# Kernel tuning notes

Measured on AMD Instinct MI355X. Metric: run time of the kernel, lower is better.

Reference implementation:

```python
import jax, jax.numpy as jnp
import numpy as np

N_NODES = 16384   # n_nodes
N_LINKS = 8192    # batch of target links
D_EMB = 128       # embedding dim
EDGE_P = 0.004    # adjacency density -> avg degree ~65


def setup_inputs() -> dict:
    key = jax.random.key(0)
    k1, k2, k3 = jax.random.split(key, 3)
    adj = jax.random.bernoulli(k1, EDGE_P, (N_NODES, N_NODES))
    adj = adj | adj.T                      # symmetric graph
    adj = adj & ~jnp.eye(N_NODES, dtype=bool)  # no self loops
    links = jax.random.randint(k2, (N_LINKS, 2), 0, N_NODES)
    emb = jax.random.normal(k3, (N_NODES, D_EMB), dtype=jnp.float32)
    return {"targetLink": links, "adjacent": adj, "NodeEmbedding": emb}


def reference(targetLink, adjacent, NodeEmbedding):
    # targetLink: [B,2] int, adjacent: [N,N] bool, NodeEmbedding: [N,D] float
    i = targetLink[:, 0]
    j = targetLink[:, 1]
    emb_i = NodeEmbedding[i]               # [B,D] gather
    emb_j = NodeEmbedding[j]               # [B,D] gather
    product = emb_i * emb_j                # [B,D]
    # common-neighbor indicator: u is a CN of (i,j) iff adj[i,u] and adj[j,u]
    cn_mask = (adjacent[i] & adjacent[j]).astype(NodeEmbedding.dtype)  # [B,N]
    # sum of embeddings over common neighbors (fused gather-reduce)
    cn_sum = cn_mask @ NodeEmbedding       # [B,D]
    return jnp.concatenate([product, cn_sum], axis=-1)  # [B,2D]
```

## Files before the change

kernel.cpp:

```cpp
#include <hip/hip_runtime.h>

#define N_NODES 16384
#define D_EMB   128
#define LIST_CAP 1024

__global__ __launch_bounds__(256) void detect_layout_kernel(
    const unsigned int* __restrict__ words, int* __restrict__ flag)
{
    __shared__ int s_any;
    if (threadIdx.x == 0) s_any = 0;
    __syncthreads();
    int any = 0;
    for (int k = threadIdx.x; k < 16384; k += 256) {
        if (words[k] > 1u) any = 1;
    }
    if (any) atomicOr(&s_any, 1);
    __syncthreads();
    if (threadIdx.x == 0) *flag = s_any;
}

__global__ __launch_bounds__(256) void ncn_kernel(
    const int* __restrict__ links,
    const void* __restrict__ adjv,
    const float* __restrict__ emb,
    float* __restrict__ out,
    const int* __restrict__ flag,
    int n_links)
{
    const int link = blockIdx.x;
    if (link >= n_links) return;

    const int i = links[2 * link];
    const int j = links[2 * link + 1];

    __shared__ int s_list[LIST_CAP];
    __shared__ int s_count;
    if (threadIdx.x == 0) s_count = 0;
    __syncthreads();

    const int byte_layout = flag ? flag[0] : 1;

    if (byte_layout) {
        const uint4* rowi = reinterpret_cast<const uint4*>(
            (const unsigned char*)adjv + (size_t)i * N_NODES);
        const uint4* rowj = reinterpret_cast<const uint4*>(
            (const unsigned char*)adjv + (size_t)j * N_NODES);
#pragma unroll
        for (int c = 0; c < 4; ++c) {
            const int idx = c * 256 + threadIdx.x;
            const uint4 a = rowi[idx];
            const uint4 b = rowj[idx];
            unsigned int m[4];
            m[0] = a.x & b.x; m[1] = a.y & b.y; m[2] = a.z & b.z; m[3] = a.w & b.w;
            if (m[0] | m[1] | m[2] | m[3]) {
                const int base = idx * 16;
#pragma unroll
                for (int w = 0; w < 4; ++w) {
                    unsigned int v = m[w];
                    if (!v) continue;
#pragma unroll
                    for (int b8 = 0; b8 < 4; ++b8) {
                        if ((v >> (8 * b8)) & 0xFFu) {
                            int pos = atomicAdd(&s_count, 1);
                            if (pos < LIST_CAP) s_list[pos] = base + w * 4 + b8;
                        }
                    }
                }
            }
        }
    } else {
        const uint4* rowi = reinterpret_cast<const uint4*>(
            (const int*)adjv + (size_t)i * N_NODES);
        const uint4* rowj = reinterpret_cast<const uint4*>(
            (const int*)adjv + (size_t)j * N_NODES);
#pragma unroll
        for (int c = 0; c < 16; ++c) {
            const int idx = c * 256 + threadIdx.x;
            const uint4 a = rowi[idx];
            const uint4 b = rowj[idx];
            const int base = idx * 4;
            if (a.x & b.x) { int p = atomicAdd(&s_count, 1); if (p < LIST_CAP) s_list[p] = base + 0; }
            if (a.y & b.y) { int p = atomicAdd(&s_count, 1); if (p < LIST_CAP) s_list[p] = base + 1; }
            if (a.z & b.z) { int p = atomicAdd(&s_count, 1); if (p < LIST_CAP) s_list[p] = base + 2; }
            if (a.w & b.w) { int p = atomicAdd(&s_count, 1); if (p < LIST_CAP) s_list[p] = base + 3; }
        }
    }
    __syncthreads();

    int count = s_count;
    if (count > LIST_CAP) count = LIST_CAP;

    const int t = threadIdx.x;
    const size_t obase = (size_t)link * (2 * D_EMB);
    if (t < D_EMB) {
        const float ei = emb[(size_t)i * D_EMB + t];
        const float ej = emb[(size_t)j * D_EMB + t];
        out[obase + t] = ei * ej;
    } else {
        const int d = t - D_EMB;
        float s = 0.0f;
        for (int c = 0; c < count; ++c) {
            s += emb[(size_t)s_list[c] * D_EMB + d];
        }
        out[obase + D_EMB + d] = s;
    }
}

extern "C" void kernel_launch(void* const* d_in, const int* in_sizes, int n_in,
                              void* d_out, int out_size, void* d_ws, size_t ws_size,
                              hipStream_t stream) {
    const int* links = (const int*)d_in[0];
    const void* adj = d_in[1];
    const float* emb = (const float*)d_in[2];
    float* out = (float*)d_out;

    const int n_links = in_sizes[0] / 2;

    int* flag = (ws_size >= sizeof(int)) ? (int*)d_ws : nullptr;
    if (flag) {
        detect_layout_kernel<<<1, 256, 0, stream>>>((const unsigned int*)adj, flag);
    }
    ncn_kernel<<<n_links, 256, 0, stream>>>(links, adj, emb, out, flag, n_links);
}
```

Before: 178.8 us.

## Compress referenced adjacency rows to bitmaps before per-link intersection

Adds a preprocessing pipeline: mark which nodes appear as link endpoints, compress only those adjacency rows into 512-word bitmaps in workspace, then intersect bitmaps per link using ffs to enumerate common neighbors. This aims to cut the repeated full-row adjacency reads (each endpoint row is reused across many links) down to a single read per distinct row plus small bitmap reads. It adds three extra kernel launches and needs about 32 MB of workspace. When the workspace is too small it falls back to the direct kernel, whose default layout now assumes int storage.

```diff
diff --git a/kernel.cpp b/kernel.cpp
--- a/kernel.cpp
+++ b/kernel.cpp
@@ -3,33 +3,91 @@
 #define N_NODES 16384
 #define D_EMB   128
 #define LIST_CAP 1024
-
-__global__ __launch_bounds__(256) void detect_layout_kernel(
-    const unsigned int* __restrict__ words, int* __restrict__ flag)
-{
-    __shared__ int s_any;
-    if (threadIdx.x == 0) s_any = 0;
-    __syncthreads();
-    int any = 0;
-    for (int k = threadIdx.x; k < 16384; k += 256) {
-        if (words[k] > 1u) any = 1;
-    }
-    if (any) atomicOr(&s_any, 1);
-    __syncthreads();
-    if (threadIdx.x == 0) *flag = s_any;
-}
-
-__global__ __launch_bounds__(256) void ncn_kernel(
-    const int* __restrict__ links,
-    const void* __restrict__ adjv,
-    const float* __restrict__ emb,
-    float* __restrict__ out,
-    const int* __restrict__ flag,
-    int n_links)
+#define BM_WORDS 512
+#define FLAG_OFF N_NODES
+#define BM_OFF_BYTES (1 << 17)
+#define WS_NEEDED (BM_OFF_BYTES + (size_t)N_NODES * (BM_WORDS * 4))
+
+__global__ __launch_bounds__(256) void zero_probe_kernel(
+    const unsigned int* __restrict__ words, int* __restrict__ flags)
+{
+    const int idx = blockIdx.x * 256 + threadIdx.x;
+    flags[idx] = 0;
+    if (blockIdx.x == 0) {
+        __shared__ int s_any;
+        if (threadIdx.x == 0) s_any = 0;
+        __syncthreads();
+        int any = 0;
+        for (int k = threadIdx.x; k < 16384; k += 256)
+            if (words[k] > 1u) any = 1;
+        if (any) atomicOr(&s_any, 1);
+        __syncthreads();
+        if (threadIdx.x == 0) flags[FLAG_OFF] = s_any;
+    }
+}
+
+__global__ __launch_bounds__(256) void mark_kernel(
+    const int* __restrict__ links, int* __restrict__ flags, int n_endpoints)
+{
+    const int k = blockIdx.x * 256 + threadIdx.x;
+    if (k < n_endpoints) flags[links[k]] = 1;
+}
+
+__global__ __launch_bounds__(256) void compress_kernel(
+    const void* __restrict__ adjv, const int* __restrict__ flags,
+    unsigned int* __restrict__ bm)
+{
+    const int r = blockIdx.x;
+    if (!flags[r]) return;
+    const int byte_layout = flags[FLAG_OFF];
+    unsigned int* dst = bm + (size_t)r * BM_WORDS;
+
+    if (!byte_layout) {
+        const uint4* row = reinterpret_cast<const uint4*>(
+            (const int*)adjv + (size_t)r * N_NODES);
+#pragma unroll
+        for (int half = 0; half < 2; ++half) {
+            const int w = threadIdx.x * 2 + half;
+            unsigned int bits = 0;
+#pragma unroll
+            for (int k = 0; k < 8; ++k) {
+                const uint4 v = row[w * 8 + k];
+                bits |= (v.x ? 1u : 0u) << (k * 4 + 0);
+                bits |= (v.y ? 1u : 0u) << (k * 4 + 1);
+                bits |= (v.z ? 1u : 0u) << (k * 4 + 2);
+                bits |= (v.w ? 1u : 0u) << (k * 4 + 3);
+            }
+            dst[w] = bits;
+        }
+    } else {
+        const uint4* row = reinterpret_cast<const uint4*>(
+            (const unsigned char*)adjv + (size_t)r * N_NODES);
+#pragma unroll
+        for (int half = 0; half < 2; ++half) {
+            const int w = threadIdx.x * 2 + half;
+            unsigned int bits = 0;
+#pragma unroll
+            for (int q = 0; q < 2; ++q) {
+                const uint4 v = row[w * 2 + q];
+                const unsigned int arr[4] = {v.x, v.y, v.z, v.w};
+#pragma unroll
+                for (int a = 0; a < 4; ++a)
+#pragma unroll
+                    for (int bb = 0; bb < 4; ++bb)
+                        bits |= ((((arr[a] >> (8 * bb)) & 0xFFu) ? 1u : 0u)
+                                 << (q * 16 + a * 4 + bb));
+            }
+            dst[w] = bits;
+        }
+    }
+}
+
+__global__ __launch_bounds__(256) void link_kernel(
+    const int* __restrict__ links, const unsigned int* __restrict__ bm,
+    const float* __restrict__ emb, float* __restrict__ out, int n_links)
 {
     const int link = blockIdx.x;
     if (link >= n_links) return;
-
     const int i = links[2 * link];
     const int j = links[2 * link + 1];
 
@@ -38,8 +96,67 @@
     if (threadIdx.x == 0) s_count = 0;
     __syncthreads();
 
-    const int byte_layout = flag ? flag[0] : 1;
-
+    const unsigned int* bi = bm + (size_t)i * BM_WORDS;
+    const unsigned int* bj = bm + (size_t)j * BM_WORDS;
+#pragma unroll
+    for (int h = 0; h < 2; ++h) {
+        const int w = h * 256 + threadIdx.x;
+        unsigned int m = bi[w] & bj[w];
+        while (m) {
+            const int b = __ffs(m) - 1;
+            m &= m - 1;
+            const int pos = atomicAdd(&s_count, 1);
+            if (pos < LIST_CAP) s_list[pos] = w * 32 + b;
+        }
+    }
+    __syncthreads();
+
+    int count = s_count;
+    if (count > LIST_CAP) count = LIST_CAP;
+
+    const int t = threadIdx.x;
+    const size_t obase = (size_t)link * (2 * D_EMB);
+    if (t < D_EMB) {
+        out[obase + t] = emb[(size_t)i * D_EMB + t] * emb[(size_t)j * D_EMB + t];
+    } else {
+        const int d = t - D_EMB;
+        float s = 0.0f;
+        for (int c = 0; c < count; ++c)
+            s += emb[(size_t)s_list[c] * D_EMB + d];
+        out[obase + D_EMB + d] = s;
+    }
+}
+
+__global__ __launch_bounds__(256) void detect_layout_kernel(
+    const unsigned int* __restrict__ words, int* __restrict__ flag)
+{
+    __shared__ int s_any;
+    if (threadIdx.x == 0) s_any = 0;
+    __syncthreads();
+    int any = 0;
+    for (int k = threadIdx.x; k < 16384; k += 256)
+        if (words[k] > 1u) any = 1;
+    if (any) atomicOr(&s_any, 1);
+    __syncthreads();
+    if (threadIdx.x == 0) *flag = s_any;
+}
+
+__global__ __launch_bounds__(256) void ncn_direct(
+    const int* __restrict__ links, const void* __restrict__ adjv,
+    const float* __restrict__ emb, float* __restrict__ out,
+    const int* __restrict__ flag, int n_links)
+{
+    const int link = blockIdx.x;
+    if (link >= n_links) return;
+    const int i = links[2 * link];
+    const int j = links[2 * link + 1];
+
+    __shared__ int s_list[LIST_CAP];
+    __shared__ int s_count;
+    if (threadIdx.x == 0) s_count = 0;
+    __syncthreads();
+
+    const int byte_layout = flag ? flag[0] : 0;
     if (byte_layout) {
         const uint4* rowi = reinterpret_cast<const uint4*>(
             (const unsigned char*)adjv + (size_t)i * N_NODES);
@@ -50,8 +167,7 @@
             const int idx = c * 256 + threadIdx.x;
             const uint4 a = rowi[idx];
             const uint4 b = rowj[idx];
-            unsigned int m[4];
-            m[0] = a.x & b.x; m[1] = a.y & b.y; m[2] = a.z & b.z; m[3] = a.w & b.w;
+            unsigned int m[4] = {a.x & b.x, a.y & b.y, a.z & b.z, a.w & b.w};
             if (m[0] | m[1] | m[2] | m[3]) {
                 const int base = idx * 16;
 #pragma unroll
@@ -93,15 +209,12 @@
     const int t = threadIdx.x;
     const size_t obase = (size_t)link * (2 * D_EMB);
     if (t < D_EMB) {
-        const float ei = emb[(size_t)i * D_EMB + t];
-        const float ej = emb[(size_t)j * D_EMB + t];
-        out[obase + t] = ei * ej;
+        out[obase + t] = emb[(size_t)i * D_EMB + t] * emb[(size_t)j * D_EMB + t];
     } else {
         const int d = t - D_EMB;
         float s = 0.0f;
-        for (int c = 0; c < count; ++c) {
+        for (int c = 0; c < count; ++c)
             s += emb[(size_t)s_list[c] * D_EMB + d];
-        }
         out[obase + D_EMB + d] = s;
     }
 }
@@ -116,9 +229,19 @@
 
     const int n_links = in_sizes[0] / 2;
 
-    int* flag = (ws_size >= sizeof(int)) ? (int*)d_ws : nullptr;
-    if (flag) {
-        detect_layout_kernel<<<1, 256, 0, stream>>>((const unsigned int*)adj, flag);
-    }
-    ncn_kernel<<<n_links, 256, 0, stream>>>(links, adj, emb, out, flag, n_links);
-}
+    if (ws_size >= WS_NEEDED) {
+        int* flags = (int*)d_ws;
+        unsigned int* bm = (unsigned int*)((char*)d_ws + BM_OFF_BYTES);
+        zero_probe_kernel<<<N_NODES / 256, 256, 0, stream>>>(
+            (const unsigned int*)adj, flags);
+        mark_kernel<<<(2 * n_links + 255) / 256, 256, 0, stream>>>(
+            links, flags, 2 * n_links);
+        compress_kernel<<<N_NODES, 256, 0, stream>>>(adj, flags, bm);
+        link_kernel<<<n_links, 256, 0, stream>>>(links, bm, emb, out, n_links);
+    } else {
+        int* flag = (ws_size >= sizeof(int)) ? (int*)d_ws : nullptr;
+        if (flag) detect_layout_kernel<<<1, 256, 0, stream>>>(
+            (const unsigned int*)adj, flag);
+        ncn_direct<<<n_links, 256, 0, stream>>>(links, adj, emb, out, flag, n_links);
+    }
+}
```

After: 220.2 us. 23.2% more time.
